# Optimization experiments

Measured on AMD Instinct MI355X. Metric: run time of the kernel, lower is better.

The kernel has to match this reference:

```python
import jax, jax.numpy as jnp
import numpy as np

B, T, C, H = 8, 2048, 1024, 64  # batch, seq_len(block_size), embedding_size, head_size


def setup_inputs() -> dict:
    key = jax.random.key(0)
    kx, kk, kq, kv = jax.random.split(key, 4)
    x = jax.random.normal(kx, (B, T, C), dtype=jnp.float32)
    # nn.Linear(C, H, bias=False) weights, stored as [in, out] for x @ W
    s = 1.0 / np.sqrt(C)
    Wk = jax.random.uniform(kk, (C, H), dtype=jnp.float32, minval=-s, maxval=s)
    Wq = jax.random.uniform(kq, (C, H), dtype=jnp.float32, minval=-s, maxval=s)
    Wv = jax.random.uniform(kv, (C, H), dtype=jnp.float32, minval=-s, maxval=s)
    return {"x": x, "Wk": Wk, "Wq": Wq, "Wv": Wv}


def reference(x, Wk, Wq, Wv):
    Bx, Tx, Cx = x.shape
    k = jnp.einsum('btc,ch->bth', x, Wk)
    q = jnp.einsum('btc,ch->bth', x, Wq)
    v = jnp.einsum('btc,ch->bth', x, Wv)
    # NOTE: original scales by embedding dim C ** -0.5, not head_size
    scores = jnp.einsum('bth,bsh->bts', q, k) * (Cx ** -0.5)  # [B,T,T]
    causal = jnp.tril(jnp.ones((Tx, Tx), dtype=bool))
    scores = jnp.where(causal, scores, -jnp.inf)
    attn = jax.nn.softmax(scores, axis=-1)
    # dropout is identity in eval/deterministic mode
    out = jnp.einsum('bts,bsh->bth', attn, v)  # [B,T,H]
    return out
```

## Files before the change

### kernel.cpp

```cpp
#include <hip/hip_runtime.h>
#include <hip/hip_bf16.h>
#include <math.h>


#define BT 16384
#define TSEQ 2048
#define XST 72

typedef __attribute__((ext_vector_type(8))) __bf16 bf16x8;
typedef __attribute__((ext_vector_type(8))) unsigned short ushort8;
typedef __attribute__((ext_vector_type(4))) float floatx4;

#define MFMA16(a, b, c) __builtin_amdgcn_mfma_f32_16x16x32_bf16( \
    __builtin_bit_cast(bf16x8, (a)), __builtin_bit_cast(bf16x8, (b)), (c), 0, 0, 0)

__device__ inline unsigned short f2bf(float f) {
  unsigned u = __builtin_bit_cast(unsigned, f);
  u += 0x7FFFu + ((u >> 16) & 1u);
  return (unsigned short)(u >> 16);
}
__device__ inline float bf2f(unsigned short s) {
  return __builtin_bit_cast(float, (unsigned)s << 16);
}
__device__ inline unsigned long long pack4bf(floatx4 f) {
  return (unsigned long long)f2bf(f[0]) | ((unsigned long long)f2bf(f[1]) << 16) |
         ((unsigned long long)f2bf(f[2]) << 32) | ((unsigned long long)f2bf(f[3]) << 48);
}
__device__ inline void glds16(const unsigned short* g, unsigned short* l) {
  __builtin_amdgcn_global_load_lds(
      (const __attribute__((address_space(1))) unsigned int*)g,
      (__attribute__((address_space(3))) unsigned int*)l, 16, 0, 0);
}

__global__ __launch_bounds__(256) void wt2_kernel(
    const float* __restrict__ Wq, const float* __restrict__ Wk,
    const float* __restrict__ Wv, unsigned short* __restrict__ Wt2) {
  __shared__ float ls[64][65];
  const int m = blockIdx.x >> 4;
  const int kci = blockIdx.x & 15;
  const int c0 = kci << 6;
  const float* __restrict__ W = (m == 0) ? Wq : (m == 1) ? Wk : Wv;
  const int tid = threadIdx.x;
#pragma unroll
  for (int i = 0; i < 16; ++i) {
    int idx = tid + (i << 8);
    int cl = idx >> 6, h = idx & 63;
    ls[cl][h] = W[(c0 + cl) * 64 + h];
  }
  __syncthreads();
  const int w = tid >> 6, lane = tid & 63;
  const int quad = lane >> 4, l16 = lane & 15;
  const int nt = (m << 2) + w;
#pragma unroll
  for (int half = 0; half < 2; ++half) {
    ushort8 t;
#pragma unroll
    for (int j = 0; j < 8; ++j)
      t[j] = f2bf(ls[(half << 5) + (quad << 3) + j][(w << 4) + l16]);
    *(ushort8*)(Wt2 + ((size_t)(((nt << 4) + kci) * 2 + half) << 9) +
                (lane << 3)) = t;
  }
}

#define XB16 1152

__global__ __launch_bounds__(256, 4) void qkv_mfma(
    const float* __restrict__ x, const unsigned short* __restrict__ Wt2,
    unsigned short* __restrict__ Qf, unsigned short* __restrict__ Kf,
    unsigned short* __restrict__ Vf) {
  __shared__ __align__(16) unsigned short smem[3840];

  const int tid = threadIdx.x;
  const int w = tid >> 6, lane = tid & 63;
  const int quad = lane >> 4, l16 = lane & 15;
  const int r0 = blockIdx.x << 4;
  const int xrow = tid >> 4;
  const int xcol = (tid & 15) << 2;
  const float* __restrict__ xp = x + (size_t)(r0 + xrow) * 1024 + xcol;
  const int xw = xrow * XST + xcol;
  const unsigned short* __restrict__ bbase = Wt2 + (lane << 3);

  floatx4 acc[3];
#pragma unroll
  for (int n = 0; n < 3; ++n) acc[n] = (floatx4){0.f, 0.f, 0.f, 0.f};

  floatx4 pf[4];
#pragma unroll
  for (int s = 0; s < 4; ++s) pf[s] = *(const floatx4*)(xp + (s << 6));
  ushort8 bfr[2][3][2];
#pragma unroll
  for (int n = 0; n < 3; ++n)
#pragma unroll
    for (int h = 0; h < 2; ++h)
      bfr[0][n][h] = *(const ushort8*)(bbase +
          ((size_t)(((3 * w + n) << 5) + h) << 9));
  *(unsigned long long*)&smem[xw] = pack4bf(pf[0]);
  asm volatile("s_waitcnt lgkmcnt(0)" ::: "memory");
  __builtin_amdgcn_sched_barrier(0);
  __builtin_amdgcn_s_barrier();
  __builtin_amdgcn_sched_barrier(0);

#pragma unroll
  for (int c = 0; c < 16; ++c) {
    const int cur = c & 1;
    if (c + 1 < 16)
      *(unsigned long long*)&smem[((c + 1) & 1) * XB16 + xw] =
          pack4bf(pf[(c + 1) & 3]);
    if (c + 4 < 16) pf[c & 3] = *(const floatx4*)(xp + ((c + 4) << 6));
    if (c + 1 < 16) {
#pragma unroll
      for (int n = 0; n < 3; ++n)
#pragma unroll
        for (int h = 0; h < 2; ++h)
          bfr[(c + 1) & 1][n][h] = *(const ushort8*)(bbase +
              ((size_t)((((3 * w + n) << 4) + (c + 1)) * 2 + h) << 9));
    }
    ushort8 af[2];
#pragma unroll
    for (int h = 0; h < 2; ++h)
      af[h] = *(const ushort8*)&smem[cur * XB16 + l16 * XST + (h << 5) +
                                     (quad << 3)];
#pragma unroll
    for (int h = 0; h < 2; ++h)
#pragma unroll
      for (int n = 0; n < 3; ++n)
        acc[n] = MFMA16(af[h], bfr[cur][n][h], acc[n]);

    asm volatile("s_waitcnt lgkmcnt(0)" ::: "memory");
    __builtin_amdgcn_sched_barrier(0);
    __builtin_amdgcn_s_barrier();
    __builtin_amdgcn_sched_barrier(0);
  }

#pragma unroll
  for (int i = 0; i < 3; ++i) {
    const int nt = 3 * w + i;
    const int m = nt >> 2, hg = nt & 3;
    if (m < 2) {
#pragma unroll
      for (int r = 0; r < 4; ++r)
        smem[m * XB16 + ((quad << 2) + r) * XST + (hg << 4) + l16] =
            f2bf(acc[i][r]);
    } else {
      *(unsigned long long*)&smem[2304 + ((hg << 4) + l16) * 24 + (quad << 2)] =
          pack4bf(acc[i]);
    }
  }
  __syncthreads();

  const int b = r0 >> 11;
  const int r16 = (r0 & 2047) >> 4;
  const int st = (r0 & 2047) >> 6;
  const int ntK = (r0 >> 4) & 3;
  const int khV = (r0 >> 5) & 1;
  const int q0v = (r0 >> 3) & 3;
#pragma unroll
  for (int i = 0; i < 2; ++i) {
    const int f = (w << 1) + i;
    if (f < 2) {
      const int kh = f;
      ushort8 t = *(const ushort8*)&smem[l16 * XST + (kh << 5) + (quad << 3)];
      *(ushort8*)(Qf + ((((size_t)b * 128 + r16) * 2 + kh) << 9) +
                  (lane << 3)) = t;
    } else if (f < 4) {
      const int kh = f - 2;
      ushort8 t = *(const ushort8*)&smem[XB16 + l16 * XST + (kh << 5) +
                                         (quad << 3)];
      *(ushort8*)(Kf + ((((size_t)(b * 32 + st) * 4 + ntK) * 2 + kh) << 9) +
                  (lane << 3)) = t;
    } else {
      const int ntE = f - 4;
      if ((quad >> 1) == (q0v >> 1)) {
        ushort8 t = *(const ushort8*)&smem[2304 + ((ntE << 4) + l16) * 24 +
                                           ((quad - q0v) << 3)];
        *(ushort8*)(Vf + ((((size_t)(b * 32 + st) * 4 + ntE) * 2 + khV) << 9) +
                    (lane << 3)) = t;
      }
    }
  }
}

__global__ __launch_bounds__(256, 3) void attn_part(
    const unsigned short* __restrict__ Qf, const unsigned short* __restrict__ Kf,
    const unsigned short* __restrict__ Vf, float* __restrict__ part) {
  __shared__ __align__(16) unsigned short KV[2][8192];
  __shared__ unsigned short Pw[4][16 * XST];

  const int tid = threadIdx.x;
  const int w = tid >> 6, lane = tid & 63;
  const int quad = lane >> 4, l16 = lane & 15;
  const int b = blockIdx.x / 144;
  const int e = blockIdx.x - b * 144;
  int g = 0;
#pragma unroll
  for (int gg = 1; gg < 8; ++gg) g += (e >= 2 * gg * (gg + 1)) ? 1 : 0;
  const int rem2 = e - 2 * g * (g + 1);
  const int qt = (g << 2) + rem2 / (g + 1);
  const int ch = rem2 - (rem2 / (g + 1)) * (g + 1);
  const int s0 = ch << 2;
  const int s1 = (s0 + 4 < qt + 1) ? s0 + 4 : qt + 1;
  const int r16 = (qt << 2) + w;

#define KVIDX(ss, nt, kh) \
  (((((size_t)(b * 32 + (ss)) << 2) + (nt)) * 2 + (kh)) << 9)
#define STAGE_KV(ss, db)                                                     \
  {                                                                          \
    _Pragma("unroll") for (int r_ = 0; r_ < 4; ++r_) {                       \
      const int f_ = (r_ << 2) + w;                                          \
      const unsigned short* src_ =                                           \
          (f_ < 8) ? Kf + KVIDX(ss, (f_ >> 1), (f_ & 1)) + (lane << 3)       \
                   : Vf + KVIDX(ss, (f_ >> 1) - 4, (f_ & 1)) + (lane << 3);  \
      glds16(src_, &KV[db][f_ << 9]);                                        \
    }                                                                        \
  }

  const unsigned short* qbase =
      Qf + ((((size_t)b * 128 + r16) * 2) << 9) + (lane << 3);
  ushort8 qf0 = *(const ushort8*)qbase;
  ushort8 qf1 = *(const ushort8*)(qbase + 512);
  __builtin_amdgcn_sched_barrier(0);

  STAGE_KV(s0, 0);
  __builtin_amdgcn_sched_barrier(0);
  STAGE_KV((s0 + 1 < s1) ? s0 + 1 : s1 - 1, 1);
  __builtin_amdgcn_sched_barrier(0);
  asm volatile("s_waitcnt vmcnt(4)");
  __builtin_amdgcn_sched_barrier(0);
  __builtin_amdgcn_s_barrier();
  __builtin_amdgcn_sched_barrier(0);

  floatx4 acc[4], lacc;
#pragma unroll
  for (int nt = 0; nt < 4; ++nt) acc[nt] = (floatx4){0.f, 0.f, 0.f, 0.f};
  lacc = (floatx4){0.f, 0.f, 0.f, 0.f};
  const ushort8 ones = {0x3F80, 0x3F80, 0x3F80, 0x3F80,
                        0x3F80, 0x3F80, 0x3F80, 0x3F80};

  for (int s = s0; s < s1; ++s) {
    const int cur = (s - s0) & 1;
    ushort8 bk[4][2], bv[4][2];
#pragma unroll
    for (int nt = 0; nt < 4; ++nt)
#pragma unroll
      for (int kh = 0; kh < 2; ++kh) {
        bk[nt][kh] = *(const ushort8*)&KV[cur][((((nt << 1) + kh)) << 9) +
                                              (lane << 3)];
        bv[nt][kh] = *(const ushort8*)&KV[cur][(((8 + (nt << 1) + kh)) << 9) +
                                              (lane << 3)];
      }
    asm volatile("s_waitcnt lgkmcnt(0)");
    __builtin_amdgcn_sched_barrier(0);
    __builtin_amdgcn_s_barrier();
    __builtin_amdgcn_sched_barrier(0);

    STAGE_KV((s + 2 < s1) ? s + 2 : s1 - 1, cur);
    __builtin_amdgcn_sched_barrier(0);

    floatx4 sf[4];
#pragma unroll
    for (int nt = 0; nt < 4; ++nt) {
      sf[nt] = (floatx4){0.f, 0.f, 0.f, 0.f};
      sf[nt] = MFMA16(qf0, bk[nt][0], sf[nt]);
      sf[nt] = MFMA16(qf1, bk[nt][1], sf[nt]);
    }

    const bool diag = (s == qt);
    const int qrow = (w << 4) + (quad << 2);
#pragma unroll
    for (int nt = 0; nt < 4; ++nt) {
      const int keyl = (nt << 4) + l16;
#pragma unroll
      for (int r = 0; r < 4; ++r) {
        float ev = __expf(sf[nt][r] * 0.03125f);
        if (diag && keyl > qrow + r) ev = 0.f;
        Pw[w][((quad << 2) + r) * XST + keyl] = f2bf(ev);
      }
    }

#pragma unroll
    for (int kh = 0; kh < 2; ++kh) {
      ushort8 pa = *(const ushort8*)&Pw[w][l16 * XST + (kh << 5) + (quad << 3)];
      lacc = MFMA16(pa, ones, lacc);
#pragma unroll
      for (int nt = 0; nt < 4; ++nt) acc[nt] = MFMA16(pa, bv[nt][kh], acc[nt]);
    }

    __builtin_amdgcn_sched_barrier(0);
    asm volatile("s_waitcnt vmcnt(4)");
    __builtin_amdgcn_sched_barrier(0);
    __builtin_amdgcn_s_barrier();
    __builtin_amdgcn_sched_barrier(0);
  }
#undef STAGE_KV
#undef KVIDX

  float* slot = part + (size_t)(b * 144 + e) * 2112;
  if (l16 == 0) {
#pragma unroll
    for (int r = 0; r < 4; ++r) slot[(w << 4) + (quad << 2) + r] = lacc[r];
  }
  unsigned short* op = (unsigned short*)(slot + 64);
#pragma unroll
  for (int nt = 0; nt < 4; ++nt)
#pragma unroll
    for (int r = 0; r < 4; ++r)
      op[((w << 4) + (quad << 2) + r) * 64 + (nt << 4) + l16] = f2bf(acc[nt][r]);
}

__global__ __launch_bounds__(256) void attn_combine(
    const float* __restrict__ part, float* __restrict__ out) {
  const int rh = blockIdx.x & 1;
  const int bqt = blockIdx.x >> 1;
  const int b = bqt >> 5, qt = bqt & 31;
  const int tid = threadIdx.x;
  const int row = (rh << 5) + (tid >> 3);
  const int hseg = (tid & 7) << 3;
  const int g = qt >> 2;
  const int nch = g + 1;
  const int ebase = 2 * g * (g + 1) + (qt & 3) * (g + 1);

  float l = 0.f;
  float ov[8];
#pragma unroll
  for (int i = 0; i < 8; ++i) ov[i] = 0.f;
  for (int c = 0; c < nch; ++c) {
    const float* slot = part + (size_t)(b * 144 + ebase + c) * 2112;
    l += slot[row];
    ushort8 o0 = *(const ushort8*)((const unsigned short*)(slot + 64) +
                                   row * 64 + hseg);
#pragma unroll
    for (int i = 0; i < 8; ++i) ov[i] += bf2f(o0[i]);
  }
  const float inv = 1.f / l;
  float* o = out + ((size_t)(b * TSEQ + (qt << 6) + row)) * 64 + hseg;
#pragma unroll
  for (int i = 0; i < 8; ++i) o[i] = ov[i] * inv;
}

extern "C" void kernel_launch(void* const* d_in, const int* in_sizes, int n_in,
                              void* d_out, int out_size, void* d_ws, size_t ws_size,
                              hipStream_t stream) {
  const float* x  = (const float*)d_in[0];
  const float* Wk = (const float*)d_in[1];
  const float* Wq = (const float*)d_in[2];
  const float* Wv = (const float*)d_in[3];

  unsigned short* Qfw = (unsigned short*)d_ws;
  unsigned short* Kfw = Qfw + (size_t)BT * 64;
  unsigned short* Vfw = Kfw + (size_t)BT * 64;
  unsigned short* Wt2 = Vfw + (size_t)BT * 64;
  float* part = (float*)(Wt2 + 3 * 64 * 1024);

  wt2_kernel<<<48, 256, 0, stream>>>(Wq, Wk, Wv, Wt2);
  qkv_mfma<<<1024, 256, 0, stream>>>(x, Wt2, Qfw, Kfw, Vfw);
  attn_part<<<1152, 256, 0, stream>>>(Qfw, Kfw, Vfw, part);
  attn_combine<<<512, 256, 0, stream>>>(part, (float*)d_out);
}
```

Baseline: 139.8 us.

## Load x directly into MFMA A-fragments, dropping LDS staging and barriers

In the QKV projection kernel, each lane now loads its own x rows from global memory straight into registers in MFMA A-operand layout and converts them to bf16 in place. This removes the LDS round-trip and the per-chunk workgroup barriers, with a two-deep register prefetch of x. The cost is that every one of the four waves loads the same x tile (4x redundant global/L2 traffic) and uses more registers, so launch bounds drop occupancy from 4 to 3 blocks per CU.

```diff
diff --git a/kernel.cpp b/kernel.cpp
--- a/kernel.cpp
+++ b/kernel.cpp
@@ -25,6 +25,14 @@
 __device__ inline unsigned long long pack4bf(floatx4 f) {
   return (unsigned long long)f2bf(f[0]) | ((unsigned long long)f2bf(f[1]) << 16) |
          ((unsigned long long)f2bf(f[2]) << 32) | ((unsigned long long)f2bf(f[3]) << 48);
+}
+__device__ inline ushort8 pack8bf(floatx4 a, floatx4 b) {
+  ushort8 t;
+#pragma unroll
+  for (int i = 0; i < 4; ++i) t[i] = f2bf(a[i]);
+#pragma unroll
+  for (int i = 0; i < 4; ++i) t[4 + i] = f2bf(b[i]);
+  return t;
 }
 __device__ inline void glds16(const unsigned short* g, unsigned short* l) {
   __builtin_amdgcn_global_load_lds(
@@ -64,7 +72,7 @@
 
 #define XB16 1152
 
-__global__ __launch_bounds__(256, 4) void qkv_mfma(
+__global__ __launch_bounds__(256, 3) void qkv_mfma(
     const float* __restrict__ x, const unsigned short* __restrict__ Wt2,
     unsigned short* __restrict__ Qf, unsigned short* __restrict__ Kf,
     unsigned short* __restrict__ Vf) {
@@ -74,62 +82,58 @@
   const int w = tid >> 6, lane = tid & 63;
   const int quad = lane >> 4, l16 = lane & 15;
   const int r0 = blockIdx.x << 4;
-  const int xrow = tid >> 4;
-  const int xcol = (tid & 15) << 2;
-  const float* __restrict__ xp = x + (size_t)(r0 + xrow) * 1024 + xcol;
-  const int xw = xrow * XST + xcol;
+  const float* __restrict__ xp = x + (size_t)(r0 + l16) * 1024 + (quad << 3);
   const unsigned short* __restrict__ bbase = Wt2 + (lane << 3);
 
   floatx4 acc[3];
 #pragma unroll
   for (int n = 0; n < 3; ++n) acc[n] = (floatx4){0.f, 0.f, 0.f, 0.f};
 
-  floatx4 pf[4];
-#pragma unroll
-  for (int s = 0; s < 4; ++s) pf[s] = *(const floatx4*)(xp + (s << 6));
+  floatx4 pf[2][2][2];
+#pragma unroll
+  for (int h = 0; h < 2; ++h)
+#pragma unroll
+    for (int p = 0; p < 2; ++p) {
+      pf[0][h][p] = *(const floatx4*)(xp + (h << 5) + (p << 2));
+      pf[1][h][p] = *(const floatx4*)(xp + 64 + (h << 5) + (p << 2));
+    }
   ushort8 bfr[2][3][2];
 #pragma unroll
   for (int n = 0; n < 3; ++n)
 #pragma unroll
     for (int h = 0; h < 2; ++h)
       bfr[0][n][h] = *(const ushort8*)(bbase +
-          ((size_t)(((3 * w + n) << 5) + h) << 9));
-  *(unsigned long long*)&smem[xw] = pack4bf(pf[0]);
-  asm volatile("s_waitcnt lgkmcnt(0)" ::: "memory");
-  __builtin_amdgcn_sched_barrier(0);
-  __builtin_amdgcn_s_barrier();
-  __builtin_amdgcn_sched_barrier(0);
+          ((size_t)((((3 * w + n) << 4) + 0) * 2 + h) << 9));
 
 #pragma unroll
   for (int c = 0; c < 16; ++c) {
     const int cur = c & 1;
-    if (c + 1 < 16)
-      *(unsigned long long*)&smem[((c + 1) & 1) * XB16 + xw] =
-          pack4bf(pf[(c + 1) & 3]);
-    if (c + 4 < 16) pf[c & 3] = *(const floatx4*)(xp + ((c + 4) << 6));
+    ushort8 af[2];
+    af[0] = pack8bf(pf[cur][0][0], pf[cur][0][1]);
+    af[1] = pack8bf(pf[cur][1][0], pf[cur][1][1]);
+    __builtin_amdgcn_sched_barrier(0);
+    if (c + 2 < 16) {
+#pragma unroll
+      for (int h = 0; h < 2; ++h)
+#pragma unroll
+        for (int p = 0; p < 2; ++p)
+          pf[cur][h][p] =
+              *(const floatx4*)(xp + ((c + 2) << 6) + (h << 5) + (p << 2));
+    }
     if (c + 1 < 16) {
 #pragma unroll
       for (int n = 0; n < 3; ++n)
 #pragma unroll
         for (int h = 0; h < 2; ++h)
-          bfr[(c + 1) & 1][n][h] = *(const ushort8*)(bbase +
+          bfr[cur ^ 1][n][h] = *(const ushort8*)(bbase +
               ((size_t)((((3 * w + n) << 4) + (c + 1)) * 2 + h) << 9));
     }
-    ushort8 af[2];
-#pragma unroll
-    for (int h = 0; h < 2; ++h)
-      af[h] = *(const ushort8*)&smem[cur * XB16 + l16 * XST + (h << 5) +
-                                     (quad << 3)];
+    __builtin_amdgcn_sched_barrier(0);
 #pragma unroll
     for (int h = 0; h < 2; ++h)
 #pragma unroll
       for (int n = 0; n < 3; ++n)
         acc[n] = MFMA16(af[h], bfr[cur][n][h], acc[n]);
-
-    asm volatile("s_waitcnt lgkmcnt(0)" ::: "memory");
-    __builtin_amdgcn_sched_barrier(0);
-    __builtin_amdgcn_s_barrier();
-    __builtin_amdgcn_sched_barrier(0);
   }
 
 #pragma unroll
```

After: 153.1 us. +9.5%, slower.

## Tile QKV projection over 32 rows and stage weights in LDS via direct global loads

Applied to the files above, without the earlier changes.

The QKV projection kernel now handles 32 rows per block with 512 threads in place of 16 rows with 256. Weight tiles are loaded straight into shared memory with global-to-LDS loads (glds16) and double-buffered, so eight waves share each weight tile instead of each wave fetching its own fragments from global memory. This halves weight traffic per output row and drops the per-wave B-register double buffer. In exchange, shared memory per block grows a lot, which may limit how many blocks fit per CU, and the vmcnt waits are hand-tuned, so they must match the exact number of outstanding loads.

```diff
diff --git a/kernel.cpp b/kernel.cpp
--- a/kernel.cpp
+++ b/kernel.cpp
@@ -62,120 +62,139 @@
   }
 }
 
-#define XB16 1152
-
-__global__ __launch_bounds__(256, 4) void qkv_mfma(
+#define XQ9 2304
+#define BB9 4608
+#define BS9 12288
+
+__global__ __launch_bounds__(512, 4) void qkv_mfma(
     const float* __restrict__ x, const unsigned short* __restrict__ Wt2,
     unsigned short* __restrict__ Qf, unsigned short* __restrict__ Kf,
     unsigned short* __restrict__ Vf) {
-  __shared__ __align__(16) unsigned short smem[3840];
+  __shared__ __align__(16) unsigned short smem[29184];
 
   const int tid = threadIdx.x;
   const int w = tid >> 6, lane = tid & 63;
   const int quad = lane >> 4, l16 = lane & 15;
-  const int r0 = blockIdx.x << 4;
+  const int wr = w >> 2, wn = w & 3;
+  const int r0 = blockIdx.x << 5;
   const int xrow = tid >> 4;
   const int xcol = (tid & 15) << 2;
   const float* __restrict__ xp = x + (size_t)(r0 + xrow) * 1024 + xcol;
   const int xw = xrow * XST + xcol;
-  const unsigned short* __restrict__ bbase = Wt2 + (lane << 3);
 
   floatx4 acc[3];
 #pragma unroll
   for (int n = 0; n < 3; ++n) acc[n] = (floatx4){0.f, 0.f, 0.f, 0.f};
 
   floatx4 pf[4];
+
+#pragma unroll
+  for (int i = 0; i < 3; ++i) {
+    const int f = 3 * w + i;
+    glds16(Wt2 + ((size_t)(((f >> 1) << 4) * 2 + (f & 1)) << 9) + (lane << 3),
+           &smem[BB9 + (f << 9)]);
+  }
+  __builtin_amdgcn_sched_barrier(0);
 #pragma unroll
   for (int s = 0; s < 4; ++s) pf[s] = *(const floatx4*)(xp + (s << 6));
-  ushort8 bfr[2][3][2];
-#pragma unroll
-  for (int n = 0; n < 3; ++n)
+  __builtin_amdgcn_sched_barrier(0);
+  *(unsigned long long*)&smem[xw] = pack4bf(pf[0]);
+  __builtin_amdgcn_sched_barrier(0);
+  asm volatile("s_waitcnt vmcnt(3)");
+  asm volatile("s_waitcnt lgkmcnt(0)");
+  __builtin_amdgcn_sched_barrier(0);
+  __builtin_amdgcn_s_barrier();
+  __builtin_amdgcn_sched_barrier(0);
+
+#pragma unroll
+  for (int c = 0; c < 16; ++c) {
+    if (c + 1 < 16)
+      *(unsigned long long*)&smem[((c + 1) & 1) * XQ9 + xw] =
+          pack4bf(pf[(c + 1) & 3]);
+    __builtin_amdgcn_sched_barrier(0);
+    if (c + 1 < 16) {
+#pragma unroll
+      for (int i = 0; i < 3; ++i) {
+        const int f = 3 * w + i;
+        glds16(Wt2 + ((size_t)((((f >> 1) << 4) + (c + 1)) * 2 + (f & 1)) << 9) +
+                   (lane << 3),
+               &smem[BB9 + ((c + 1) & 1) * BS9 + (f << 9)]);
+      }
+    }
+    __builtin_amdgcn_sched_barrier(0);
+    if (c + 4 < 16) pf[(c + 4) & 3] = *(const floatx4*)(xp + ((c + 4) << 6));
+    __builtin_amdgcn_sched_barrier(0);
+
+    ushort8 af[2];
 #pragma unroll
     for (int h = 0; h < 2; ++h)
-      bfr[0][n][h] = *(const ushort8*)(bbase +
-          ((size_t)(((3 * w + n) << 5) + h) << 9));
-  *(unsigned long long*)&smem[xw] = pack4bf(pf[0]);
-  asm volatile("s_waitcnt lgkmcnt(0)" ::: "memory");
-  __builtin_amdgcn_sched_barrier(0);
-  __builtin_amdgcn_s_barrier();
-  __builtin_amdgcn_sched_barrier(0);
-
-#pragma unroll
-  for (int c = 0; c < 16; ++c) {
-    const int cur = c & 1;
-    if (c + 1 < 16)
-      *(unsigned long long*)&smem[((c + 1) & 1) * XB16 + xw] =
-          pack4bf(pf[(c + 1) & 3]);
-    if (c + 4 < 16) pf[c & 3] = *(const floatx4*)(xp + ((c + 4) << 6));
-    if (c + 1 < 16) {
+      af[h] = *(const ushort8*)&smem[(c & 1) * XQ9 + ((wr << 4) + l16) * XST +
+                                     (h << 5) + (quad << 3)];
+    ushort8 bfr[3][2];
+#pragma unroll
+    for (int n = 0; n < 3; ++n)
+#pragma unroll
+      for (int h = 0; h < 2; ++h)
+        bfr[n][h] = *(const ushort8*)&smem[BB9 + (c & 1) * BS9 +
+            ((((3 * wn + n) << 1) + h) << 9) + (lane << 3)];
+#pragma unroll
+    for (int h = 0; h < 2; ++h)
 #pragma unroll
       for (int n = 0; n < 3; ++n)
-#pragma unroll
-        for (int h = 0; h < 2; ++h)
-          bfr[(c + 1) & 1][n][h] = *(const ushort8*)(bbase +
-              ((size_t)((((3 * w + n) << 4) + (c + 1)) * 2 + h) << 9));
-    }
-    ushort8 af[2];
-#pragma unroll
-    for (int h = 0; h < 2; ++h)
-      af[h] = *(const ushort8*)&smem[cur * XB16 + l16 * XST + (h << 5) +
-                                     (quad << 3)];
-#pragma unroll
-    for (int h = 0; h < 2; ++h)
-#pragma unroll
-      for (int n = 0; n < 3; ++n)
-        acc[n] = MFMA16(af[h], bfr[cur][n][h], acc[n]);
-
-    asm volatile("s_waitcnt lgkmcnt(0)" ::: "memory");
+        acc[n] = MFMA16(af[h], bfr[n][h], acc[n]);
+
+    __builtin_amdgcn_sched_barrier(0);
+    if (c <= 11) { asm volatile("s_waitcnt vmcnt(1)"); }
+    else         { asm volatile("s_waitcnt vmcnt(0)"); }
+    asm volatile("s_waitcnt lgkmcnt(0)");
     __builtin_amdgcn_sched_barrier(0);
     __builtin_amdgcn_s_barrier();
     __builtin_amdgcn_sched_barrier(0);
   }
 
 #pragma unroll
-  for (int i = 0; i < 3; ++i) {
-    const int nt = 3 * w + i;
+  for (int n = 0; n < 3; ++n) {
+    const int nt = 3 * wn + n;
     const int m = nt >> 2, hg = nt & 3;
     if (m < 2) {
 #pragma unroll
       for (int r = 0; r < 4; ++r)
-        smem[m * XB16 + ((quad << 2) + r) * XST + (hg << 4) + l16] =
-            f2bf(acc[i][r]);
+        smem[m * XQ9 + ((wr << 4) + (quad << 2) + r) * XST + (hg << 4) + l16] =
+            f2bf(acc[n][r]);
     } else {
-      *(unsigned long long*)&smem[2304 + ((hg << 4) + l16) * 24 + (quad << 2)] =
-          pack4bf(acc[i]);
+      *(unsigned long long*)&smem[4608 + ((hg << 4) + l16) * XST + (wr << 4) +
+                                  (quad << 2)] = pack4bf(acc[n]);
     }
   }
   __syncthreads();
 
   const int b = r0 >> 11;
-  const int r16 = (r0 & 2047) >> 4;
+  const int r16b = (r0 & 2047) >> 4;
   const int st = (r0 & 2047) >> 6;
-  const int ntK = (r0 >> 4) & 3;
+  const int ntKb = (r0 >> 4) & 3;
   const int khV = (r0 >> 5) & 1;
-  const int q0v = (r0 >> 3) & 3;
 #pragma unroll
   for (int i = 0; i < 2; ++i) {
-    const int f = (w << 1) + i;
-    if (f < 2) {
-      const int kh = f;
-      ushort8 t = *(const ushort8*)&smem[l16 * XST + (kh << 5) + (quad << 3)];
-      *(ushort8*)(Qf + ((((size_t)b * 128 + r16) * 2 + kh) << 9) +
+    const int f = (i == 0) ? w : (w + 8);
+    if (i == 1 && w >= 4) break;
+    if (f < 4) {
+      const int grpL = f >> 1, kh = f & 1;
+      ushort8 t = *(const ushort8*)&smem[((grpL << 4) + l16) * XST +
+                                         (kh << 5) + (quad << 3)];
+      *(ushort8*)(Qf + ((((size_t)b * 128 + r16b + grpL) * 2 + kh) << 9) +
                   (lane << 3)) = t;
-    } else if (f < 4) {
-      const int kh = f - 2;
-      ushort8 t = *(const ushort8*)&smem[XB16 + l16 * XST + (kh << 5) +
-                                         (quad << 3)];
-      *(ushort8*)(Kf + ((((size_t)(b * 32 + st) * 4 + ntK) * 2 + kh) << 9) +
+    } else if (f < 8) {
+      const int g2 = (f - 4) >> 1, kh = f & 1;
+      ushort8 t = *(const ushort8*)&smem[XQ9 + ((g2 << 4) + l16) * XST +
+                                         (kh << 5) + (quad << 3)];
+      *(ushort8*)(Kf + ((((size_t)(b * 32 + st) * 4 + ntKb + g2) * 2 + kh) << 9) +
                   (lane << 3)) = t;
     } else {
-      const int ntE = f - 4;
-      if ((quad >> 1) == (q0v >> 1)) {
-        ushort8 t = *(const ushort8*)&smem[2304 + ((ntE << 4) + l16) * 24 +
-                                           ((quad - q0v) << 3)];
-        *(ushort8*)(Vf + ((((size_t)(b * 32 + st) * 4 + ntE) * 2 + khV) << 9) +
-                    (lane << 3)) = t;
-      }
+      const int ntE = f - 8;
+      ushort8 t = *(const ushort8*)&smem[4608 + ((ntE << 4) + l16) * XST +
+                                         (quad << 3)];
+      *(ushort8*)(Vf + ((((size_t)(b * 32 + st) * 4 + ntE) * 2 + khV) << 9) +
+                  (lane << 3)) = t;
     }
   }
 }
@@ -352,7 +371,7 @@
   float* part = (float*)(Wt2 + 3 * 64 * 1024);
 
   wt2_kernel<<<48, 256, 0, stream>>>(Wq, Wk, Wv, Wt2);
-  qkv_mfma<<<1024, 256, 0, stream>>>(x, Wt2, Qfw, Kfw, Vfw);
+  qkv_mfma<<<512, 512, 0, stream>>>(x, Wt2, Qfw, Kfw, Vfw);
   attn_part<<<1152, 256, 0, stream>>>(Qfw, Kfw, Vfw, part);
   attn_combine<<<512, 256, 0, stream>>>(part, (float*)d_out);
 }
```

Result: faster. 132.8 us (-5.0%).
